# Kernel tuning notes

Hardware: AMD Instinct MI355X
Metric: run time of the kernel (lower is better)

## Reference

```python
import jax, jax.numpy as jnp
import numpy as np
import math

B, S, H = 2, 2048, 4096
N_HEADS, HEAD_DIM = 32, 128
ROPE_THETA = 10000.0


def _rope_tables(seq_len, head_dim, dtype):
    inv_freq = 1.0 / (ROPE_THETA ** (jnp.arange(0, head_dim, 2, dtype=jnp.float32) / head_dim))
    t = jnp.arange(seq_len, dtype=jnp.float32)
    freqs = jnp.outer(t, inv_freq)                    # [S, D/2]
    emb = jnp.concatenate([freqs, freqs], axis=-1)    # [S, D]
    return jnp.cos(emb).astype(dtype), jnp.sin(emb).astype(dtype)


def _rotate_half(x):
    d = x.shape[-1] // 2
    return jnp.concatenate([-x[..., d:], x[..., :d]], axis=-1)


def setup_inputs() -> dict:
    key = jax.random.key(0)
    k0, k1, k2, k3, k4 = jax.random.split(key, 5)
    hidden_states = jax.random.normal(k0, (B, S, H), dtype=jnp.float32)
    # additive causal mask: 0 on/below diagonal, -1e9 above
    causal = jnp.triu(jnp.full((S, S), -1e9, dtype=jnp.float32), k=1)
    attention_mask = jnp.broadcast_to(causal, (B, 1, S, S))
    # BitNet b1.58 ternary weights {-1,0,1} with per-layer scalar scale
    wq = jax.random.randint(k1, (H, H), -1, 2).astype(jnp.float32)
    wk = jax.random.randint(k2, (H, H), -1, 2).astype(jnp.float32)
    wv = jax.random.randint(k3, (H, H), -1, 2).astype(jnp.float32)
    wo = jax.random.randint(k4, (H, H), -1, 2).astype(jnp.float32)
    scale = jnp.float32(0.02)
    return {"hidden_states": hidden_states, "attention_mask": attention_mask,
            "wq": wq, "wk": wk, "wv": wv, "wo": wo,
            "sq": scale, "sk": scale, "sv": scale, "so": scale}


def reference(hidden_states, attention_mask, wq, wk, wv, wo, sq, sk, sv, so):
    bsz, q_len, _ = hidden_states.shape
    dtype = hidden_states.dtype

    def qlin(x, w, s):  # QuantizedLinear: x @ (w_ternary * scale)^T
        return jnp.einsum('bsh,oh->bso', x, w) * s

    def split_heads(x):  # [B,S,H] -> [B,nH,S,D]
        return x.reshape(bsz, q_len, N_HEADS, HEAD_DIM).transpose(0, 2, 1, 3)

    q = split_heads(qlin(hidden_states, wq, sq))
    k = split_heads(qlin(hidden_states, wk, sk))
    v = split_heads(qlin(hidden_states, wv, sv))

    cos, sin = _rope_tables(q_len, HEAD_DIM, dtype)   # [S, D]
    q = q * cos + _rotate_half(q) * sin
    k = k * cos + _rotate_half(k) * sin

    scores = jnp.einsum('bnqd,bnkd->bnqk', q, k) / math.sqrt(HEAD_DIM)
    scores = scores + attention_mask
    scores = jnp.maximum(scores, jnp.finfo(scores.dtype).min)
    attn = jax.nn.softmax(scores, axis=-1)
    out = jnp.einsum('bnqk,bnkd->bnqd', attn, v)       # [B,nH,S,D]
    out = out.transpose(0, 2, 1, 3).reshape(bsz, q_len, N_HEADS * HEAD_DIM)
    return jnp.einsum('bsh,oh->bso', out, wo) * so
```

## Files before the change

### kernel.cpp

```cpp
#include <hip/hip_runtime.h>
#include <stdint.h>
#include <math.h>


#define HDIM   4096
#define SEQ    2048
#define NBATCH 2
#define NROWS  (NBATCH * SEQ)
#define NHEADS 32
#define DHEAD  128
#define QBLK   128

typedef __attribute__((ext_vector_type(8))) short short8;
typedef __attribute__((ext_vector_type(4))) short short4v;
typedef __attribute__((ext_vector_type(4))) float f32x4;
typedef unsigned short u16;
typedef unsigned int   u32;

__device__ __forceinline__ float bf2f(u16 u) {
  union { float f; u32 i; } x; x.i = ((u32)u) << 16; return x.f;
}
__device__ __forceinline__ u16 f2bf(float f) {
  union { float f; u32 i; } x; x.f = f;
  u32 r = x.i + 0x7FFFu + ((x.i >> 16) & 1u);
  return (u16)(r >> 16);
}

__device__ __forceinline__ void gload16(const u16* g, u16* l) {
  __builtin_amdgcn_global_load_lds(
      (const __attribute__((address_space(1))) u32*)g,
      (__attribute__((address_space(3))) u32*)l, 16, 0, 0);
}

__device__ __forceinline__ void unpack2(u32 v, float& a, float& b) {
  a = bf2f((u16)(v & 0xffffu)); b = bf2f((u16)(v >> 16));
}
__device__ __forceinline__ u32 pack2(float a, float b) {
  return (u32)f2bf(a) | ((u32)f2bf(b) << 16);
}

__global__ void f2bf_vec(const float* __restrict__ in, u16* __restrict__ out, int n4) {
  int i = blockIdx.x * blockDim.x + threadIdx.x;
  const int stride = gridDim.x * blockDim.x;
  for (; i < n4; i += stride) {
    float4 v = reinterpret_cast<const float4*>(in)[i];
    u32 lo = (u32)f2bf(v.x) | ((u32)f2bf(v.y) << 16);
    u32 hi = (u32)f2bf(v.z) | ((u32)f2bf(v.w) << 16);
    reinterpret_cast<uint2*>(out)[i] = make_uint2(lo, hi);
  }
}

__global__ void rope_tables_k(float* __restrict__ cosT, float* __restrict__ sinT) {
  int idx = blockIdx.x * blockDim.x + threadIdx.x;
  if (idx >= SEQ * 64) return;
  int s = idx >> 6, d = idx & 63;
  float ex = (float)(2 * d) / 128.0f;
  float inv = powf(10000.0f, -ex);
  float f = (float)s * inv;
  cosT[idx] = cosf(f);
  sinT[idx] = sinf(f);
}

__global__ void rope_apply(u16* __restrict__ Q, u16* __restrict__ K,
                           const float* __restrict__ cosT, const float* __restrict__ sinT) {
  const int row = blockIdx.x;
  u16* T = (blockIdx.y == 0) ? Q : K;
  const int pos = row & (SEQ - 1);
  for (int i = threadIdx.x; i < NHEADS * 16; i += blockDim.x) {
    const int hd = i >> 4, d0 = (i & 15) * 4;
    const size_t base = (size_t)row * HDIM + hd * DHEAD + d0;
    uint2 alo = *reinterpret_cast<const uint2*>(&T[base]);
    uint2 ahi = *reinterpret_cast<const uint2*>(&T[base + 64]);
    float4 c4 = *reinterpret_cast<const float4*>(&cosT[pos * 64 + d0]);
    float4 s4 = *reinterpret_cast<const float4*>(&sinT[pos * 64 + d0]);
    float l0, l1, l2, l3, h0, h1, h2, h3;
    unpack2(alo.x, l0, l1); unpack2(alo.y, l2, l3);
    unpack2(ahi.x, h0, h1); unpack2(ahi.y, h2, h3);
    uint2 olo, ohi;
    olo.x = pack2(l0 * c4.x - h0 * s4.x, l1 * c4.y - h1 * s4.y);
    olo.y = pack2(l2 * c4.z - h2 * s4.z, l3 * c4.w - h3 * s4.w);
    ohi.x = pack2(h0 * c4.x + l0 * s4.x, h1 * c4.y + l1 * s4.y);
    ohi.y = pack2(h2 * c4.z + l2 * s4.z, h3 * c4.w + l3 * s4.w);
    *reinterpret_cast<uint2*>(&T[base]) = olo;
    *reinterpret_cast<uint2*>(&T[base + 64]) = ohi;
  }
}

template<int OUTF>
__global__ __launch_bounds__(512, 2)
void gemm8(const u16* __restrict__ Am, const u16* __restrict__ Bm,
           void* __restrict__ Cout, const float* __restrict__ scale_ptr) {
  extern __shared__ __align__(16) u16 ldsp[];

  const int tid = threadIdx.x;
  const int w = tid >> 6, lane = tid & 63;
  const int llo = lane & 15, lhi = (lane >> 4) & 3;
  const int wr = w >> 2, wc = w & 3;

  const int bid = blockIdx.x;
  const int xcd = bid & 7, ii = bid >> 3;
  const int by = (xcd >> 1) * 4 + (ii & 3);
  const int bx = (xcd & 1) * 8 + (ii >> 2);
  const int rowBase = by * 256, colBase = bx * 256;
  const float scl = scale_ptr[0];

  auto stage_half = [&](const u16* G, int obase, int ts, int h, int opB) {
    const int p = ts & 1;
    const u32 base = (opB ? 32768u : 0u) + (u32)p * 16384u + (u32)h * 8192u;
#pragma unroll
    for (int i = 0; i < 2; ++i) {
      const int ru = i * 64 + w * 8;
      const int r = ru + (lane >> 3);
      const int cc = (lane & 7) ^ (r & 7);
      gload16(G + (size_t)(obase + h * 128 + r) * HDIM + ts * 64 + cc * 8,
              ldsp + base + (u32)ru * 64u);
    }
  };

  f32x4 acc[8][4];
#pragma unroll
  for (int m = 0; m < 8; ++m)
#pragma unroll
    for (int n = 0; n < 4; ++n) acc[m][n] = (f32x4)0.0f;

#define PH(TCUR, MH, NH, TS, H, OPB, DOSTAGE, VMN) do {                          \
    const int p_ = (TCUR) & 1;                                                   \
    short8 af_[4][2]; short8 bf_[2][2];                                          \
    const u32 ab_ = (u32)(p_ * 16384 + (MH) * 8192);                             \
    const u32 bb_ = (u32)(32768 + p_ * 16384 + (NH) * 8192);                     \
    _Pragma("unroll")                                                            \
    for (int m4 = 0; m4 < 4; ++m4) { const int r_ = wr * 64 + m4 * 16 + llo;     \
      _Pragma("unroll")                                                          \
      for (int kk = 0; kk < 2; ++kk) { const int c_ = kk * 4 + lhi;              \
        af_[m4][kk] = *reinterpret_cast<const short8*>(                          \
            ldsp + ab_ + r_ * 64 + ((c_ ^ (r_ & 7)) * 8)); } }                   \
    _Pragma("unroll")                                                            \
    for (int n2 = 0; n2 < 2; ++n2) { const int r_ = wc * 32 + n2 * 16 + llo;     \
      _Pragma("unroll")                                                          \
      for (int kk = 0; kk < 2; ++kk) { const int c_ = kk * 4 + lhi;              \
        bf_[n2][kk] = *reinterpret_cast<const short8*>(                          \
            ldsp + bb_ + r_ * 64 + ((c_ ^ (r_ & 7)) * 8)); } }                   \
    if (DOSTAGE) stage_half((OPB) ? Bm : Am, (OPB) ? colBase : rowBase,          \
                            (TS), (H), (OPB));                                   \
    __builtin_amdgcn_s_barrier();                                                \
    asm volatile("s_waitcnt lgkmcnt(0)" ::: "memory");                           \
    __builtin_amdgcn_s_setprio(1);                                               \
    _Pragma("unroll")                                                            \
    for (int m4 = 0; m4 < 4; ++m4)                                               \
      _Pragma("unroll")                                                          \
      for (int n2 = 0; n2 < 2; ++n2)                                             \
        _Pragma("unroll")                                                        \
        for (int kk = 0; kk < 2; ++kk)                                           \
          acc[(MH) * 4 + m4][(NH) * 2 + n2] =                                    \
              __builtin_amdgcn_mfma_f32_16x16x32_bf16(                           \
                  af_[m4][kk], bf_[n2][kk],                                      \
                  acc[(MH) * 4 + m4][(NH) * 2 + n2], 0, 0, 0);                   \
    __builtin_amdgcn_s_setprio(0);                                               \
    if ((VMN) == 4) asm volatile("s_waitcnt vmcnt(4)" ::: "memory");             \
    if ((VMN) == 0) asm volatile("s_waitcnt vmcnt(0)" ::: "memory");             \
    __builtin_amdgcn_s_barrier();                                                \
  } while (0)

  stage_half(Am, rowBase, 0, 0, 0);
  stage_half(Bm, colBase, 0, 0, 1);
  stage_half(Am, rowBase, 0, 1, 0);
  stage_half(Bm, colBase, 0, 1, 1);
  stage_half(Am, rowBase, 1, 0, 0);
  stage_half(Bm, colBase, 1, 0, 1);
  asm volatile("s_waitcnt vmcnt(4)" ::: "memory");
  __builtin_amdgcn_s_barrier();

  for (int it = 0; it < 31; ++it) {
    const int T = 2 * it;
    PH(T,     0, 0, T + 1, 1, 0, 1, -1);
    PH(T,     0, 1, T + 1, 1, 1, 1, -1);
    PH(T,     1, 0, T + 2, 0, 0, 1, -1);
    PH(T,     1, 1, T + 2, 0, 1, 1,  4);
    PH(T + 1, 0, 0, T + 2, 1, 0, 1, -1);
    PH(T + 1, 0, 1, T + 2, 1, 1, 1, -1);
    PH(T + 1, 1, 0, T + 3, 0, 0, 1, -1);
    PH(T + 1, 1, 1, T + 3, 0, 1, 1,  4);
  }
  PH(62, 0, 0, 63, 1, 0, 1, -1);
  PH(62, 0, 1, 63, 1, 1, 1, -1);
  PH(62, 1, 0,  0, 0, 0, 0, -1);
  PH(62, 1, 1,  0, 0, 0, 0,  0);
  PH(63, 0, 0,  0, 0, 0, 0, -1);
  PH(63, 0, 1,  0, 0, 0, 0, -1);
  PH(63, 1, 0,  0, 0, 0, 0, -1);
  PH(63, 1, 1,  0, 0, 0, 0, -1);
#undef PH

#pragma unroll
  for (int mf = 0; mf < 8; ++mf)
#pragma unroll
    for (int nf = 0; nf < 4; ++nf)
#pragma unroll
      for (int r = 0; r < 4; ++r) {
        const int row = rowBase + (mf >> 2) * 128 + wr * 64 + (mf & 3) * 16 + lhi * 4 + r;
        const int col = colBase + (nf >> 1) * 128 + wc * 32 + (nf & 1) * 16 + llo;
        const float v = acc[mf][nf][r] * scl;
        if (OUTF) reinterpret_cast<float*>(Cout)[(size_t)row * HDIM + col] = v;
        else      reinterpret_cast<u16*>(Cout)[(size_t)row * HDIM + col] = f2bf(v);
      }
}

__global__ __launch_bounds__(512, 4)
void attn_causal(const u16* __restrict__ Q, const u16* __restrict__ K,
                 const u16* __restrict__ VT, u16* __restrict__ O) {
  __shared__ __align__(16) u16 Ks[2][64][128];
  __shared__ __align__(16) u16 Vt[128][72];
  __shared__ __align__(16) u16 Pw[8][16][76];

  const int tid = threadIdx.x;
  const int w = tid >> 6, lane = tid & 63;
  const int lhi = lane >> 4, llo = lane & 15;
  const int bh = blockIdx.y, b = bh >> 5, h = bh & 31;

  const u16* Kg = K + ((size_t)b * SEQ) * HDIM + h * DHEAD;
  const u16* VTg = VT + (size_t)(h * DHEAD) * NROWS + b * SEQ;

  const int krr[2] = { (tid >> 4), 32 + (tid >> 4) };
  const int kcp = tid & 15;
  const int vd = tid >> 2, vko = tid & 3;

  const float smul = 0.08838834764831845f;
  int buf = 0;

  auto issueK = [&](int kv0, int bsel) {
#pragma unroll
    for (int i = 0; i < 2; ++i) {
      const int r = krr[i];
      const int cs = kcp ^ (r & 7);
      gload16(Kg + (size_t)(kv0 + r) * HDIM + cs * 8,
              &Ks[bsel][i * 32 + (tid >> 4) & 31][0] - ((tid >> 4) & 31) * 128 + ((size_t)0));
    }
  };
  (void)issueK;

  for (int halfq = 0; halfq < 2; ++halfq) {
    const int xq = (halfq == 0) ? (int)blockIdx.x : 15 - (int)blockIdx.x;
    const int qb = xq * QBLK;
    const int ntile = qb / 64 + 2;
    const int wmax = qb + w * 16 + 15;

    const u16* Qg = Q + ((size_t)(b * SEQ + qb)) * HDIM + h * DHEAD;
    short8 qf[4];
#pragma unroll
    for (int dc = 0; dc < 4; ++dc)
      qf[dc] = *reinterpret_cast<const short8*>(Qg + (size_t)(w * 16 + llo) * HDIM + dc * 32 + lhi * 8);

    f32x4 o[8];
#pragma unroll
    for (int dt = 0; dt < 8; ++dt) o[dt] = (f32x4)0.0f;
    float mrow[4], lrow[4];
#pragma unroll
    for (int r = 0; r < 4; ++r) { mrow[r] = -__builtin_inff(); lrow[r] = 0.0f; }

    {
      u16* dst = &Ks[buf][0][0] + tid * 8;
#pragma unroll
      for (int i = 0; i < 2; ++i) {
        const int r = i * 32 + (tid >> 4);
        const int cs = kcp ^ (r & 7);
        gload16(Kg + (size_t)r * HDIM + cs * 8, dst + i * 4096);
      }
    }
    short8 vreg0 = *reinterpret_cast<const short8*>(VTg + (size_t)vd * NROWS + vko * 8);
    short8 vreg1 = *reinterpret_cast<const short8*>(VTg + (size_t)vd * NROWS + 32 + vko * 8);

    for (int t = 0; t < ntile; ++t) {
      const int kv0 = t * 64;
      __syncthreads();
      *reinterpret_cast<short8*>(&Vt[vd][vko * 8]) = vreg0;
      *reinterpret_cast<short8*>(&Vt[vd][32 + vko * 8]) = vreg1;
      __syncthreads();
      if (t + 1 < ntile) {
        const int nkv = kv0 + 64;
        u16* dst = &Ks[buf ^ 1][0][0] + tid * 8;
#pragma unroll
        for (int i = 0; i < 2; ++i) {
          const int r = i * 32 + (tid >> 4);
          const int cs = kcp ^ (r & 7);
          gload16(Kg + (size_t)(nkv + r) * HDIM + cs * 8, dst + i * 4096);
        }
        vreg0 = *reinterpret_cast<const short8*>(VTg + (size_t)vd * NROWS + nkv + vko * 8);
        vreg1 = *reinterpret_cast<const short8*>(VTg + (size_t)vd * NROWS + nkv + 32 + vko * 8);
      }

      if (kv0 <= wmax) {
        f32x4 sacc[4];
#pragma unroll
        for (int nt2 = 0; nt2 < 4; ++nt2) sacc[nt2] = (f32x4)0.0f;
        __builtin_amdgcn_s_setprio(1);
#pragma unroll
        for (int nt2 = 0; nt2 < 4; ++nt2) {
          const int r = nt2 * 16 + llo;
#pragma unroll
          for (int dc = 0; dc < 4; ++dc) {
            const int cs = (dc * 4 + lhi) ^ (r & 7);
            const short8 kf = *reinterpret_cast<const short8*>(&Ks[buf][r][cs * 8]);
            sacc[nt2] = __builtin_amdgcn_mfma_f32_16x16x32_bf16(qf[dc], kf, sacc[nt2], 0, 0, 0);
          }
        }
        __builtin_amdgcn_s_setprio(0);

        float sv[4][4];
#pragma unroll
        for (int nt2 = 0; nt2 < 4; ++nt2)
#pragma unroll
          for (int r = 0; r < 4; ++r) {
            const int kcol = kv0 + nt2 * 16 + llo;
            const int qrow = qb + w * 16 + lhi * 4 + r;
            const float xv = sacc[nt2][r] * smul;
            sv[nt2][r] = (kcol <= qrow) ? xv : -__builtin_inff();
          }
        float rmax[4];
#pragma unroll
        for (int r = 0; r < 4; ++r)
          rmax[r] = fmaxf(fmaxf(sv[0][r], sv[1][r]), fmaxf(sv[2][r], sv[3][r]));
#pragma unroll
        for (int xm = 1; xm < 16; xm <<= 1)
#pragma unroll
          for (int r = 0; r < 4; ++r) rmax[r] = fmaxf(rmax[r], __shfl_xor(rmax[r], xm));
        float p[4][4], fac[4], rsum[4];
#pragma unroll
        for (int r = 0; r < 4; ++r) {
          const float mn = fmaxf(mrow[r], rmax[r]);
          fac[r] = __expf(mrow[r] - mn);
          mrow[r] = mn;
          p[0][r] = __expf(sv[0][r] - mn);
          p[1][r] = __expf(sv[1][r] - mn);
          p[2][r] = __expf(sv[2][r] - mn);
          p[3][r] = __expf(sv[3][r] - mn);
          rsum[r] = (p[0][r] + p[1][r]) + (p[2][r] + p[3][r]);
        }
#pragma unroll
        for (int xm = 1; xm < 16; xm <<= 1)
#pragma unroll
          for (int r = 0; r < 4; ++r) rsum[r] += __shfl_xor(rsum[r], xm);
#pragma unroll
        for (int r = 0; r < 4; ++r) lrow[r] = lrow[r] * fac[r] + rsum[r];
#pragma unroll
        for (int dt = 0; dt < 8; ++dt)
#pragma unroll
          for (int r = 0; r < 4; ++r) o[dt][r] *= fac[r];

#pragma unroll
        for (int nt2 = 0; nt2 < 4; ++nt2)
#pragma unroll
          for (int r = 0; r < 4; ++r)
            Pw[w][lhi * 4 + r][nt2 * 16 + llo] = f2bf(p[nt2][r]);

        union { short4v hh[2]; short8 v8; } pu[2];
#pragma unroll
        for (int s = 0; s < 2; ++s) {
          pu[s].hh[0] = *reinterpret_cast<const short4v*>(&Pw[w][llo][s * 32 + lhi * 8]);
          pu[s].hh[1] = *reinterpret_cast<const short4v*>(&Pw[w][llo][s * 32 + lhi * 8 + 4]);
        }
        __builtin_amdgcn_s_setprio(1);
#pragma unroll
        for (int dt = 0; dt < 8; ++dt)
#pragma unroll
          for (int s = 0; s < 2; ++s) {
            const short8 vf = *reinterpret_cast<const short8*>(&Vt[dt * 16 + llo][s * 32 + lhi * 8]);
            o[dt] = __builtin_amdgcn_mfma_f32_16x16x32_bf16(pu[s].v8, vf, o[dt], 0, 0, 0);
          }
        __builtin_amdgcn_s_setprio(0);
      }
      buf ^= 1;
    }

    u16* Og = O + ((size_t)(b * SEQ + qb)) * HDIM + h * DHEAD;
    float inv[4];
#pragma unroll
    for (int r = 0; r < 4; ++r) inv[r] = 1.0f / lrow[r];
#pragma unroll
    for (int dt = 0; dt < 8; ++dt)
#pragma unroll
      for (int r = 0; r < 4; ++r)
        Og[(size_t)(w * 16 + lhi * 4 + r) * HDIM + dt * 16 + llo] = f2bf(o[dt][r] * inv[r]);
  }
}

extern "C" void kernel_launch(void* const* d_in, const int* in_sizes, int n_in,
                              void* d_out, int out_size, void* d_ws, size_t ws_size,
                              hipStream_t stream) {
  (void)in_sizes; (void)n_in; (void)out_size; (void)ws_size;
  const float* hs = (const float*)d_in[0];
  const float* wq = (const float*)d_in[2];
  const float* wk = (const float*)d_in[3];
  const float* wv = (const float*)d_in[4];
  const float* wo = (const float*)d_in[5];
  const float* sq = (const float*)d_in[6];
  const float* sk = (const float*)d_in[7];
  const float* sv = (const float*)d_in[8];
  const float* so = (const float*)d_in[9];

  char* p = (char*)d_ws;
  const size_t MAT = (size_t)NROWS * HDIM * sizeof(u16);
  u16* Xb = (u16*)p; p += MAT;
  u16* Wb = (u16*)p; p += MAT;
  u16* Qb = (u16*)p; p += MAT;
  u16* Kb = (u16*)p; p += MAT;
  u16* Vb = (u16*)p; p += MAT;
  float* cosT = (float*)p; p += (size_t)SEQ * 64 * sizeof(float);
  float* sinT = (float*)p; p += (size_t)SEQ * 64 * sizeof(float);

  const int n4 = NROWS * (HDIM / 4);
  const dim3 cb(256);
  const int LDSZ = 131072;
  (void)hipFuncSetAttribute(reinterpret_cast<const void*>(&gemm8<0>),
                            hipFuncAttributeMaxDynamicSharedMemorySize, LDSZ);
  (void)hipFuncSetAttribute(reinterpret_cast<const void*>(&gemm8<1>),
                            hipFuncAttributeMaxDynamicSharedMemorySize, LDSZ);

  f2bf_vec<<<dim3(2048), cb, 0, stream>>>(hs, Xb, n4);
  rope_tables_k<<<dim3((SEQ * 64 + 255) / 256), cb, 0, stream>>>(cosT, sinT);

  f2bf_vec<<<dim3(2048), cb, 0, stream>>>(wq, Wb, n4);
  gemm8<0><<<dim3(256), dim3(512), LDSZ, stream>>>(Xb, Wb, (void*)Qb, sq);
  f2bf_vec<<<dim3(2048), cb, 0, stream>>>(wk, Wb, n4);
  gemm8<0><<<dim3(256), dim3(512), LDSZ, stream>>>(Xb, Wb, (void*)Kb, sk);
  f2bf_vec<<<dim3(2048), cb, 0, stream>>>(wv, Wb, n4);
  gemm8<0><<<dim3(256), dim3(512), LDSZ, stream>>>(Wb, Xb, (void*)Vb, sv);

  rope_apply<<<dim3(NROWS, 2), cb, 0, stream>>>(Qb, Kb, cosT, sinT);
  attn_causal<<<dim3(8, NBATCH * NHEADS), dim3(512), 0, stream>>>(Qb, Kb, Vb, Xb);

  f2bf_vec<<<dim3(2048), cb, 0, stream>>>(wo, Wb, n4);
  gemm8<1><<<dim3(256), dim3(512), LDSZ, stream>>>(Xb, Wb, d_out, so);
}
```

Baseline: 754.5 us.

## Use exp2 softmax, lazy rescaling, skip masking off-diagonal, truncate P to bf16

Folds log2(e) into the score scale so the online softmax can use exp2f, and applies the causal mask only on tiles that cross the diagonal. It also skips the running-max update and output rescale unless some row's max has grown by more than 8 in log2 units, a FlashAttention-4-style lazy rescale. P is converted to bf16 by truncation instead of round-to-nearest, and an unused K-load lambda is removed. These cut per-tile ALU work in the softmax stage at the cost of slightly larger unnormalized exponent values and rounding bias in P.

```diff
diff --git a/kernel.cpp b/kernel.cpp
--- a/kernel.cpp
+++ b/kernel.cpp
@@ -24,6 +24,10 @@
   union { float f; u32 i; } x; x.f = f;
   u32 r = x.i + 0x7FFFu + ((x.i >> 16) & 1u);
   return (u16)(r >> 16);
+}
+__device__ __forceinline__ u16 f2bf_t(float f) {
+  union { float f; u32 i; } x; x.f = f;
+  return (u16)(x.i >> 16);
 }
 
 __device__ __forceinline__ void gload16(const u16* g, u16* l) {
@@ -220,23 +224,11 @@
   const u16* Kg = K + ((size_t)b * SEQ) * HDIM + h * DHEAD;
   const u16* VTg = VT + (size_t)(h * DHEAD) * NROWS + b * SEQ;
 
-  const int krr[2] = { (tid >> 4), 32 + (tid >> 4) };
   const int kcp = tid & 15;
   const int vd = tid >> 2, vko = tid & 3;
 
-  const float smul = 0.08838834764831845f;
+  const float smul2 = 0.127517427f;
   int buf = 0;
-
-  auto issueK = [&](int kv0, int bsel) {
-#pragma unroll
-    for (int i = 0; i < 2; ++i) {
-      const int r = krr[i];
-      const int cs = kcp ^ (r & 7);
-      gload16(Kg + (size_t)(kv0 + r) * HDIM + cs * 8,
-              &Ks[bsel][i * 32 + (tid >> 4) & 31][0] - ((tid >> 4) & 31) * 128 + ((size_t)0));
-    }
-  };
-  (void)issueK;
 
   for (int halfq = 0; halfq < 2; ++halfq) {
     const int xq = (halfq == 0) ? (int)blockIdx.x : 15 - (int)blockIdx.x;
@@ -306,15 +298,25 @@
         __builtin_amdgcn_s_setprio(0);
 
         float sv[4][4];
-#pragma unroll
-        for (int nt2 = 0; nt2 < 4; ++nt2)
-#pragma unroll
-          for (int r = 0; r < 4; ++r) {
-            const int kcol = kv0 + nt2 * 16 + llo;
-            const int qrow = qb + w * 16 + lhi * 4 + r;
-            const float xv = sacc[nt2][r] * smul;
-            sv[nt2][r] = (kcol <= qrow) ? xv : -__builtin_inff();
-          }
+        const bool dm = (kv0 + 63 > qb + w * 16);
+        if (dm) {
+#pragma unroll
+          for (int nt2 = 0; nt2 < 4; ++nt2)
+#pragma unroll
+            for (int r = 0; r < 4; ++r) {
+              const int kcol = kv0 + nt2 * 16 + llo;
+              const int qrow = qb + w * 16 + lhi * 4 + r;
+              const float xv = sacc[nt2][r] * smul2;
+              sv[nt2][r] = (kcol <= qrow) ? xv : -__builtin_inff();
+            }
+        } else {
+#pragma unroll
+          for (int nt2 = 0; nt2 < 4; ++nt2)
+#pragma unroll
+            for (int r = 0; r < 4; ++r)
+              sv[nt2][r] = sacc[nt2][r] * smul2;
+        }
+
         float rmax[4];
 #pragma unroll
         for (int r = 0; r < 4; ++r)
@@ -323,34 +325,58 @@
         for (int xm = 1; xm < 16; xm <<= 1)
 #pragma unroll
           for (int r = 0; r < 4; ++r) rmax[r] = fmaxf(rmax[r], __shfl_xor(rmax[r], xm));
-        float p[4][4], fac[4], rsum[4];
-#pragma unroll
-        for (int r = 0; r < 4; ++r) {
-          const float mn = fmaxf(mrow[r], rmax[r]);
-          fac[r] = __expf(mrow[r] - mn);
-          mrow[r] = mn;
-          p[0][r] = __expf(sv[0][r] - mn);
-          p[1][r] = __expf(sv[1][r] - mn);
-          p[2][r] = __expf(sv[2][r] - mn);
-          p[3][r] = __expf(sv[3][r] - mn);
-          rsum[r] = (p[0][r] + p[1][r]) + (p[2][r] + p[3][r]);
+
+        bool need = false;
+#pragma unroll
+        for (int r = 0; r < 4; ++r) need = need || (rmax[r] > mrow[r] + 8.0f);
+
+        float p[4][4], rsum[4];
+        if (__any(need)) {
+          float fac[4];
+#pragma unroll
+          for (int r = 0; r < 4; ++r) {
+            const float mn = fmaxf(mrow[r], rmax[r]);
+            fac[r] = exp2f(mrow[r] - mn);
+            mrow[r] = mn;
+          }
+#pragma unroll
+          for (int nt2 = 0; nt2 < 4; ++nt2)
+#pragma unroll
+            for (int r = 0; r < 4; ++r) p[nt2][r] = exp2f(sv[nt2][r] - mrow[r]);
+#pragma unroll
+          for (int r = 0; r < 4; ++r)
+            rsum[r] = (p[0][r] + p[1][r]) + (p[2][r] + p[3][r]);
+#pragma unroll
+          for (int xm = 1; xm < 16; xm <<= 1)
+#pragma unroll
+            for (int r = 0; r < 4; ++r) rsum[r] += __shfl_xor(rsum[r], xm);
+#pragma unroll
+          for (int r = 0; r < 4; ++r) lrow[r] = lrow[r] * fac[r] + rsum[r];
+#pragma unroll
+          for (int dt = 0; dt < 8; ++dt)
+#pragma unroll
+            for (int r = 0; r < 4; ++r) o[dt][r] *= fac[r];
+        } else {
+#pragma unroll
+          for (int nt2 = 0; nt2 < 4; ++nt2)
+#pragma unroll
+            for (int r = 0; r < 4; ++r) p[nt2][r] = exp2f(sv[nt2][r] - mrow[r]);
+#pragma unroll
+          for (int r = 0; r < 4; ++r)
+            rsum[r] = (p[0][r] + p[1][r]) + (p[2][r] + p[3][r]);
+#pragma unroll
+          for (int xm = 1; xm < 16; xm <<= 1)
+#pragma unroll
+            for (int r = 0; r < 4; ++r) rsum[r] += __shfl_xor(rsum[r], xm);
+#pragma unroll
+          for (int r = 0; r < 4; ++r) lrow[r] += rsum[r];
         }
-#pragma unroll
-        for (int xm = 1; xm < 16; xm <<= 1)
-#pragma unroll
-          for (int r = 0; r < 4; ++r) rsum[r] += __shfl_xor(rsum[r], xm);
-#pragma unroll
-        for (int r = 0; r < 4; ++r) lrow[r] = lrow[r] * fac[r] + rsum[r];
-#pragma unroll
-        for (int dt = 0; dt < 8; ++dt)
-#pragma unroll
-          for (int r = 0; r < 4; ++r) o[dt][r] *= fac[r];
 
 #pragma unroll
         for (int nt2 = 0; nt2 < 4; ++nt2)
 #pragma unroll
           for (int r = 0; r < 4; ++r)
-            Pw[w][lhi * 4 + r][nt2 * 16 + llo] = f2bf(p[nt2][r]);
+            Pw[w][lhi * 4 + r][nt2 * 16 + llo] = f2bf_t(p[nt2][r]);
 
         union { short4v hh[2]; short8 v8; } pu[2];
 #pragma unroll
```

Measured after the change: 1.002 ms. +32.8%, slower.
